# Kernel optimization log

Hardware: AMD Instinct MI355X
Metric: run time of the kernel (lower is better)

Reference implementation:

```python
import jax, jax.numpy as jnp
import numpy as np

B, S, D_MODEL, H = 2, 2048, 1024, 16
HD = D_MODEL // H  # 64
EPS = 1e-6


def setup_inputs() -> dict:
    key = jax.random.key(0)
    ks = jax.random.split(key, 8)
    x = jax.random.normal(ks[0], (B, S, D_MODEL), dtype=jnp.float32)
    # Proper RoPE rotation angles: theta_i = pos / 10000^(2i/head_dim)
    inv_freq = 1.0 / (10000.0 ** (np.arange(0, HD, 2, dtype=np.float32) / HD))  # (HD/2,)
    angles = np.arange(S, dtype=np.float32)[:, None] * inv_freq[None, :]        # (S, HD/2)
    rope_cos = jnp.asarray(np.cos(angles))
    rope_sin = jnp.asarray(np.sin(angles))
    w_std = 1.0 / np.sqrt(D_MODEL)
    wq = jax.random.normal(ks[1], (D_MODEL, D_MODEL), dtype=jnp.float32) * w_std
    wk = jax.random.normal(ks[2], (D_MODEL, D_MODEL), dtype=jnp.float32) * w_std
    wv = jax.random.normal(ks[3], (D_MODEL, D_MODEL), dtype=jnp.float32) * w_std
    wo = jax.random.normal(ks[4], (D_MODEL, D_MODEL), dtype=jnp.float32) * w_std
    q_scale = 1.0 + 0.02 * jax.random.normal(ks[5], (HD,), dtype=jnp.float32)
    k_scale = 1.0 + 0.02 * jax.random.normal(ks[6], (HD,), dtype=jnp.float32)
    return {"x": x, "wq": wq, "wk": wk, "wv": wv, "wo": wo,
            "q_scale": q_scale, "k_scale": k_scale,
            "rope_cos": rope_cos, "rope_sin": rope_sin}


def _rmsnorm(t, scale):
    # RMSNorm over head_dim
    var = jnp.mean(jnp.square(t), axis=-1, keepdims=True)
    return t * jax.lax.rsqrt(var + EPS) * scale


def _apply_rope(t, cos, sin):
    # t: (B,S,H,HD); interpret consecutive pairs as complex (real, imag)
    b, s, h, d = t.shape
    tp = t.reshape(b, s, h, d // 2, 2)
    tr, ti = tp[..., 0], tp[..., 1]
    c = cos[None, :, None, :]  # (1,S,1,HD/2)
    sn = sin[None, :, None, :]
    or_ = tr * c - ti * sn
    oi = tr * sn + ti * c
    return jnp.stack([or_, oi], axis=-1).reshape(b, s, h, d)


def reference(x, wq, wk, wv, wo, q_scale, k_scale, rope_cos, rope_sin):
    b, s, _ = x.shape
    # Torch-style linear: y = x @ W^T, W is (out, in)
    q = jnp.einsum('bsd,od->bso', x, wq).reshape(b, s, H, HD)
    k = jnp.einsum('bsd,od->bso', x, wk).reshape(b, s, H, HD)
    v = jnp.einsum('bsd,od->bso', x, wv).reshape(b, s, H, HD)
    q = _apply_rope(_rmsnorm(q, q_scale), rope_cos, rope_sin)
    k = _apply_rope(_rmsnorm(k, k_scale), rope_cos, rope_sin)
    # scaled dot-product attention (no mask), fp32 softmax
    scale = 1.0 / np.sqrt(HD)
    scores = jnp.einsum('bqhd,bkhd->bhqk', q, k) * scale
    probs = jax.nn.softmax(scores.astype(jnp.float32), axis=-1)
    attn = jnp.einsum('bhqk,bkhd->bqhd', probs, v).reshape(b, s, D_MODEL)
    return jnp.einsum('bso,do->bsd', attn, wo.T).astype(x.dtype) if False else jnp.einsum('bsd,od->bso', attn, wo)
```

## Files before the change

### kernel.cpp

```cpp
#include <hip/hip_runtime.h>
#include <hip/hip_bf16.h>


#define B_ 2
#define S_ 2048
#define D_ 1024
#define H_ 16
#define HD_ 64
#define M_ (B_*S_)

typedef __attribute__((ext_vector_type(8))) short short8;
typedef __attribute__((ext_vector_type(4))) short short4v;
typedef __attribute__((ext_vector_type(4))) float f32x4;
typedef __attribute__((ext_vector_type(4))) _Float16 half4;

static __device__ __forceinline__ short f2bf(float f) {
    __hip_bfloat16 h = __float2bfloat16(f);
    return *reinterpret_cast<short*>(&h);
}
static __device__ __forceinline__ short f2h(float f) {
    _Float16 h = (_Float16)f;
    return *reinterpret_cast<short*>(&h);
}
static __device__ __forceinline__ float h2f(short s) {
    _Float16 h; __builtin_memcpy(&h, &s, 2); return (float)h;
}
static __device__ __forceinline__ float bf2f(short s) {
    unsigned u = ((unsigned)(unsigned short)s) << 16;
    float f; __builtin_memcpy(&f, &u, 4); return f;
}

typedef __attribute__((address_space(1))) const unsigned int gu32_t;
typedef __attribute__((address_space(3))) unsigned int lu32_t;
static __device__ __forceinline__ void gld16(const short* g, short* l) {
    __builtin_amdgcn_global_load_lds((gu32_t*)g, (lu32_t*)l, 16, 0, 0);
}

__global__ __launch_bounds__(256)
void convert_bf16(const float* __restrict__ x,
                  const float* __restrict__ wq, const float* __restrict__ wk,
                  const float* __restrict__ wv, const float* __restrict__ wo,
                  short* __restrict__ xb, short* __restrict__ wqkvb, short* __restrict__ wob)
{
    const size_t t4 = ((size_t)blockIdx.x * 256 + threadIdx.x) * 4;
    const float* src; short* dst; size_t off, doff;
    if (t4 < 4194304)      { src = x;  dst = xb;    off = t4;           doff = t4; }
    else if (t4 < 5242880) { src = wq; dst = wqkvb; off = t4 - 4194304; doff = t4 - 4194304; }
    else if (t4 < 6291456) { src = wk; dst = wqkvb; off = t4 - 5242880; doff = t4 - 4194304; }
    else if (t4 < 7340032) { src = wv; dst = wqkvb; off = t4 - 6291456; doff = t4 - 4194304; }
    else                   { src = wo; dst = wob;   off = t4 - 7340032; doff = t4 - 7340032; }
    float4 v = *(const float4*)(src + off);
    short4v s = { f2bf(v.x), f2bf(v.y), f2bf(v.z), f2bf(v.w) };
    *(short4v*)(dst + doff) = s;
}

__global__ __launch_bounds__(256)
void gemm_qkv(const short* __restrict__ A, const short* __restrict__ Bw,
              short* __restrict__ Qb, short* __restrict__ Kb, short* __restrict__ Vt)
{
    __shared__ __align__(16) short As[128*32];
    __shared__ __align__(16) short Bs[128*32];
    const int tid = threadIdx.x;
    const int w = tid >> 6, lane = tid & 63, quad = lane >> 4, l16 = lane & 15;
    const int wr = w >> 1, wc = w & 1;
    const int bm0 = blockIdx.x * 128, bn0 = blockIdx.y * 128;

    const int srow = tid >> 2;
    const int skch = (tid & 3) * 8;
    const short* gA0 = A  + (size_t)(bm0 + srow) * 1024 + skch;
    const short* gA1 = A  + (size_t)(bm0 + 64 + srow) * 1024 + skch;
    const short* gB0 = Bw + (size_t)(bn0 + srow) * 1024 + skch;
    const short* gB1 = Bw + (size_t)(bn0 + 64 + srow) * 1024 + skch;
    short* lA0 = As + w*512;
    short* lA1 = As + 2048 + w*512;
    short* lB0 = Bs + w*512;
    short* lB1 = Bs + 2048 + w*512;

    f32x4 acc[4][4];
    #pragma unroll
    for (int i = 0; i < 4; ++i)
        #pragma unroll
        for (int j = 0; j < 4; ++j) acc[i][j] = (f32x4){0.f,0.f,0.f,0.f};

    for (int k0 = 0; k0 < 1024; k0 += 32) {
        __syncthreads();
        gld16(gA0 + k0, lA0);
        gld16(gA1 + k0, lA1);
        gld16(gB0 + k0, lB0);
        gld16(gB1 + k0, lB1);
        __syncthreads();
        short8 af[4], bfr[4];
        #pragma unroll
        for (int i = 0; i < 4; ++i)
            af[i] = *(const short8*)(As + (wr*64 + i*16 + l16)*32 + quad*8);
        #pragma unroll
        for (int j = 0; j < 4; ++j)
            bfr[j] = *(const short8*)(Bs + (wc*64 + j*16 + l16)*32 + quad*8);
        #pragma unroll
        for (int i = 0; i < 4; ++i)
            #pragma unroll
            for (int j = 0; j < 4; ++j)
                acc[i][j] = __builtin_amdgcn_mfma_f32_16x16x32_bf16(af[i], bfr[j], acc[i][j], 0, 0, 0);
    }

    #pragma unroll
    for (int i = 0; i < 4; ++i) {
        #pragma unroll
        for (int r = 0; r < 4; ++r) {
            const int m = bm0 + wr*64 + i*16 + quad*4 + r;
            #pragma unroll
            for (int j = 0; j < 4; ++j) {
                const int n = bn0 + wc*64 + j*16 + l16;
                const float v = acc[i][j][r];
                const int which = n >> 10, nn = n & 1023;
                const int h = nn >> 6, hd = nn & 63;
                const int b = m >> 11, s = m & (S_-1);
                if (which == 0)      Qb[(((size_t)b*H_ + h)*S_ + s)*HD_ + hd] = f2bf(v);
                else if (which == 1) Kb[(((size_t)b*H_ + h)*S_ + s)*HD_ + hd] = f2bf(v);
                else                 Vt[(((size_t)b*H_ + h)*HD_ + hd)*S_ + s] = f2h(v);
            }
        }
    }
}

__global__ __launch_bounds__(256)
void gemm_out(const short* __restrict__ A, const short* __restrict__ Bw,
              float* __restrict__ C)
{
    __shared__ __align__(16) short As[64*32];
    __shared__ __align__(16) short Bs[128*32];
    const int tid = threadIdx.x;
    const int w = tid >> 6, lane = tid & 63, quad = lane >> 4, l16 = lane & 15;
    const int bm0 = blockIdx.x * 64, bn0 = blockIdx.y * 128;

    const int srow = tid >> 2;
    const int skch = (tid & 3) * 8;
    const short* gA  = A  + (size_t)(bm0 + srow) * 1024 + skch;
    const short* gB0 = Bw + (size_t)(bn0 + srow) * 1024 + skch;
    const short* gB1 = Bw + (size_t)(bn0 + 64 + srow) * 1024 + skch;
    short* lA  = As + w*512;
    short* lB0 = Bs + w*512;
    short* lB1 = Bs + 2048 + w*512;

    f32x4 acc[4][2];
    #pragma unroll
    for (int i = 0; i < 4; ++i) {
        acc[i][0] = (f32x4){0.f,0.f,0.f,0.f};
        acc[i][1] = (f32x4){0.f,0.f,0.f,0.f};
    }

    for (int k0 = 0; k0 < 1024; k0 += 32) {
        __syncthreads();
        gld16(gA  + k0, lA);
        gld16(gB0 + k0, lB0);
        gld16(gB1 + k0, lB1);
        __syncthreads();
        short8 af[4], bfr[2];
        #pragma unroll
        for (int i = 0; i < 4; ++i)
            af[i] = *(const short8*)(As + (i*16 + l16)*32 + quad*8);
        #pragma unroll
        for (int j = 0; j < 2; ++j)
            bfr[j] = *(const short8*)(Bs + (w*32 + j*16 + l16)*32 + quad*8);
        #pragma unroll
        for (int i = 0; i < 4; ++i)
            #pragma unroll
            for (int j = 0; j < 2; ++j)
                acc[i][j] = __builtin_amdgcn_mfma_f32_16x16x32_bf16(af[i], bfr[j], acc[i][j], 0, 0, 0);
    }

    #pragma unroll
    for (int i = 0; i < 4; ++i)
        #pragma unroll
        for (int r = 0; r < 4; ++r) {
            const int m = bm0 + i*16 + quad*4 + r;
            #pragma unroll
            for (int j = 0; j < 2; ++j) {
                const int n = bn0 + w*32 + j*16 + l16;
                C[(size_t)m*1024 + n] = acc[i][j][r];
            }
        }
}

__global__ __launch_bounds__(256)
void rmsnorm_rope(short* __restrict__ qbh, short* __restrict__ kbh,
                  const float* __restrict__ q_scale, const float* __restrict__ k_scale,
                  const float* __restrict__ rope_cos, const float* __restrict__ rope_sin)
{
    const int lane = threadIdx.x & 63;
    const int wid  = threadIdx.x >> 6;
    const int row  = blockIdx.x * 4 + wid;
    const bool isq = (blockIdx.y == 0);
    short* t = isq ? qbh : kbh;
    const float* sc = isq ? q_scale : k_scale;
    const int s = row & (S_-1);
    float v = bf2f(t[(size_t)row * HD_ + lane]);
    float ssum = v * v;
    #pragma unroll
    for (int m = 32; m >= 1; m >>= 1) ssum += __shfl_xor(ssum, m, 64);
    float r = rsqrtf(ssum * (1.0f/64.0f) + 1e-6f);
    float nv = v * r * sc[lane];
    const int p = lane >> 1;
    float c  = rope_cos[s*32 + p];
    float sn = rope_sin[s*32 + p];
    float partner = __shfl_xor(nv, 1, 64);
    float outv = (lane & 1) ? (partner * sn + nv * c) : (nv * c - partner * sn);
    if (isq) outv *= 0.18033688011112042f;
    t[(size_t)row * HD_ + lane] = f2bf(outv);
}

__global__ __launch_bounds__(256, 2)
void flash_mfma(const short* __restrict__ qb, const short* __restrict__ kb,
                const short* __restrict__ vt, short* __restrict__ po, float* __restrict__ pl)
{
    __shared__ __align__(16) short Ks[64*64];
    __shared__ __align__(16) short Vs[64*64];

    const int tid  = threadIdx.x;
    const int wv   = tid >> 6;
    const int lane = tid & 63;
    const int quad = lane >> 4;
    const int l16  = lane & 15;
    const int bh   = blockIdx.y;
    const int b    = bh >> 4, h = bh & (H_-1);
    const int q0   = blockIdx.x * 128 + wv * 32;
    const int sp   = blockIdx.z;
    const int kt0  = sp * 1024;
    const size_t hbase = (size_t)bh * S_ * HD_;
    const size_t vbase = (size_t)bh * HD_ * S_;
    short* po_sp = po + (size_t)sp * 4194304;
    float* pl_sp = pl + (size_t)sp * 65536;

    const int c0r = tid >> 3,       c0c = tid & 7;
    const int c1r = (tid+256) >> 3, c1c = (tid+256) & 7;

    short8 qfrag[2][2];
    #pragma unroll
    for (int qf = 0; qf < 2; ++qf)
        #pragma unroll
        for (int c = 0; c < 2; ++c)
            qfrag[qf][c] = *(const short8*)(qb + hbase + (size_t)(q0 + qf*16 + l16)*HD_ + c*32 + quad*8);

    f32x4 Oacc[2][4];
    #pragma unroll
    for (int qf = 0; qf < 2; ++qf)
        #pragma unroll
        for (int dt = 0; dt < 4; ++dt) Oacc[qf][dt] = (f32x4){0.f,0.f,0.f,0.f};
    float l_lane[2] = {0.f, 0.f};

    short8 rk0 = *(const short8*)(kb + hbase + (size_t)(kt0 + c0r)*HD_ + c0c*8);
    short8 rk1 = *(const short8*)(kb + hbase + (size_t)(kt0 + c1r)*HD_ + c1c*8);
    short8 rv0 = *(const short8*)(vt + vbase + (size_t)c0r*S_ + kt0 + c0c*8);
    short8 rv1 = *(const short8*)(vt + vbase + (size_t)c1r*S_ + kt0 + c1c*8);

    #pragma unroll 1
    for (int t = 0; t < 16; ++t) {
        __syncthreads();
        *(short8*)(Ks + c0r*64 + ((c0c ^ (c0r & 7)) << 3)) = rk0;
        *(short8*)(Ks + c1r*64 + ((c1c ^ (c1r & 7)) << 3)) = rk1;
        *(short8*)(Vs + c0r*64 + ((c0c ^ (c0r & 7)) << 3)) = rv0;
        *(short8*)(Vs + c1r*64 + ((c1c ^ (c1r & 7)) << 3)) = rv1;
        __syncthreads();
        if (t < 15) {
            const int ktn = kt0 + (t+1)*64;
            rk0 = *(const short8*)(kb + hbase + (size_t)(ktn + c0r)*HD_ + c0c*8);
            rk1 = *(const short8*)(kb + hbase + (size_t)(ktn + c1r)*HD_ + c1c*8);
            rv0 = *(const short8*)(vt + vbase + (size_t)c0r*S_ + ktn + c0c*8);
            rv1 = *(const short8*)(vt + vbase + (size_t)c1r*S_ + ktn + c1c*8);
        }

        #pragma unroll
        for (int st = 0; st < 4; ++st) {
            short8 kf0 = *(const short8*)(Ks + (st*16 + l16)*64 + (((quad    ) ^ (l16 & 7)) << 3));
            short8 kf1 = *(const short8*)(Ks + (st*16 + l16)*64 + (((4 + quad) ^ (l16 & 7)) << 3));
            #pragma unroll
            for (int qf = 0; qf < 2; ++qf) {
                f32x4 acc = (f32x4){0.f,0.f,0.f,0.f};
                acc = __builtin_amdgcn_mfma_f32_16x16x32_bf16(kf0, qfrag[qf][0], acc, 0, 0, 0);
                acc = __builtin_amdgcn_mfma_f32_16x16x32_bf16(kf1, qfrag[qf][1], acc, 0, 0, 0);
                half4 pb;
                #pragma unroll
                for (int r = 0; r < 4; ++r) {
                    float p = __builtin_amdgcn_exp2f(acc[r] - 12.0f);
                    l_lane[qf] += p;
                    pb[r] = (_Float16)p;
                }
                const int ch16 = st*2 + (quad >> 1);
                const int sw   = ((ch16 ^ (l16 & 7)) << 3) + (quad & 1)*4;
                #pragma unroll
                for (int dt = 0; dt < 4; ++dt) {
                    half4 va = *(const half4*)(Vs + (dt*16 + l16)*64 + sw);
                    Oacc[qf][dt] = __builtin_amdgcn_mfma_f32_16x16x16f16(va, pb, Oacc[qf][dt], 0, 0, 0);
                }
            }
        }
    }

    #pragma unroll
    for (int qf = 0; qf < 2; ++qf) {
        l_lane[qf] += __shfl_xor(l_lane[qf], 16, 64);
        l_lane[qf] += __shfl_xor(l_lane[qf], 32, 64);
        if (quad == 0) pl_sp[(size_t)bh*S_ + q0 + qf*16 + l16] = l_lane[qf];
    }
    #pragma unroll
    for (int qf = 0; qf < 2; ++qf) {
        const int s = q0 + qf*16 + l16;
        #pragma unroll
        for (int dt = 0; dt < 4; ++dt) {
            short4v o;
            #pragma unroll
            for (int r = 0; r < 4; ++r) o[r] = f2h(Oacc[qf][dt][r]);
            *(short4v*)(po_sp + (((size_t)b*S_ + s)*H_ + h)*HD_ + dt*16 + quad*4) = o;
        }
    }
}

__global__ __launch_bounds__(256)
void flash_combine(const short* __restrict__ po, const float* __restrict__ pl,
                   short* __restrict__ attnb)
{
    const size_t idx4 = ((size_t)blockIdx.x * 256 + threadIdx.x) * 4;
    const size_t row  = idx4 >> 6;
    const int h  = (int)(row & 15);
    const size_t bs = row >> 4;
    const int b  = (int)(bs >> 11);
    const int s  = (int)(bs & (S_-1));
    const int bh = b*16 + h;
    const float l = pl[(size_t)bh*S_ + s] + pl[65536 + (size_t)bh*S_ + s];
    const float inv = 1.0f / l;
    short4v a0 = *(const short4v*)(po + idx4);
    short4v a1 = *(const short4v*)(po + 4194304 + idx4);
    short4v o;
    #pragma unroll
    for (int i = 0; i < 4; ++i) o[i] = f2bf((h2f(a0[i]) + h2f(a1[i])) * inv);
    *(short4v*)(attnb + idx4) = o;
}

extern "C" void kernel_launch(void* const* d_in, const int* in_sizes, int n_in,
                              void* d_out, int out_size, void* d_ws, size_t ws_size,
                              hipStream_t stream)
{
    (void)in_sizes; (void)n_in; (void)out_size; (void)ws_size;
    const float* x        = (const float*)d_in[0];
    const float* wq       = (const float*)d_in[1];
    const float* wk       = (const float*)d_in[2];
    const float* wv       = (const float*)d_in[3];
    const float* wo       = (const float*)d_in[4];
    const float* q_scale  = (const float*)d_in[5];
    const float* k_scale  = (const float*)d_in[6];
    const float* rope_cos = (const float*)d_in[7];
    const float* rope_sin = (const float*)d_in[8];
    float* out = (float*)d_out;
    short* ws  = (short*)d_ws;

    short* qbh   = ws;
    short* kbh   = ws + 4194304;
    short* vt    = ws + 8388608;
    short* attnb = ws + 12582912;
    short* xb    = ws + 16777216;
    short* wqkvb = ws + 20971520;
    short* wob   = ws + 24117248;
    short* po    = ws + 25165824;
    float* pl    = (float*)(ws + 33554432);

    convert_bf16<<<dim3(8192), 256, 0, stream>>>(x, wq, wk, wv, wo, xb, wqkvb, wob);
    gemm_qkv<<<dim3(M_/128, 24), 256, 0, stream>>>(xb, wqkvb, qbh, kbh, vt);
    rmsnorm_rope<<<dim3(B_*H_*S_/4, 2), 256, 0, stream>>>(qbh, kbh, q_scale, k_scale, rope_cos, rope_sin);
    flash_mfma<<<dim3(S_/128, B_*H_, 2), 256, 0, stream>>>(qbh, kbh, vt, po, pl);
    flash_combine<<<dim3(4096), 256, 0, stream>>>(po, pl, attnb);
    gemm_out<<<dim3(M_/64, D_/128), 256, 0, stream>>>(attnb, wob, out);
}
```

Measured before the change: 225.7 us.

## Fuse split-K attention combine into output projection GEMM, hoist V fragment loads

Removes the separate flash_combine kernel and folds its normalisation into gemm_out's A-tile staging. Each thread loads the two fp16 partial outputs, sums them, scales by the precomputed inverse row sums, and writes bf16 into LDS. This saves one launch and the attnb round trip through memory. The cost is that the A tile now goes through registers instead of the async global_load_lds path, and each thread does 16 pl reads per block, with the po tile re-read by every column block. In the flash kernel, the V fragments are loaded once per st and reused across both q fragments rather than reloaded per qf.

```diff
diff --git a/kernel.cpp b/kernel.cpp
--- a/kernel.cpp
+++ b/kernel.cpp
@@ -13,6 +13,7 @@
 typedef __attribute__((ext_vector_type(4))) short short4v;
 typedef __attribute__((ext_vector_type(4))) float f32x4;
 typedef __attribute__((ext_vector_type(4))) _Float16 half4;
+typedef __attribute__((ext_vector_type(8))) _Float16 half8;
 
 static __device__ __forceinline__ short f2bf(float f) {
     __hip_bfloat16 h = __float2bfloat16(f);
@@ -21,9 +22,6 @@
 static __device__ __forceinline__ short f2h(float f) {
     _Float16 h = (_Float16)f;
     return *reinterpret_cast<short*>(&h);
-}
-static __device__ __forceinline__ float h2f(short s) {
-    _Float16 h; __builtin_memcpy(&h, &s, 2); return (float)h;
 }
 static __device__ __forceinline__ float bf2f(short s) {
     unsigned u = ((unsigned)(unsigned short)s) << 16;
@@ -124,8 +122,8 @@
 }
 
 __global__ __launch_bounds__(256)
-void gemm_out(const short* __restrict__ A, const short* __restrict__ Bw,
-              float* __restrict__ C)
+void gemm_out(const short* __restrict__ po, const float* __restrict__ pl,
+              const short* __restrict__ Bw, float* __restrict__ C)
 {
     __shared__ __align__(16) short As[64*32];
     __shared__ __align__(16) short Bs[128*32];
@@ -135,12 +133,17 @@
 
     const int srow = tid >> 2;
     const int skch = (tid & 3) * 8;
-    const short* gA  = A  + (size_t)(bm0 + srow) * 1024 + skch;
+    const int m = bm0 + srow;
+    const int b = m >> 11, s = m & (S_-1);
     const short* gB0 = Bw + (size_t)(bn0 + srow) * 1024 + skch;
     const short* gB1 = Bw + (size_t)(bn0 + 64 + srow) * 1024 + skch;
-    short* lA  = As + w*512;
     short* lB0 = Bs + w*512;
     short* lB1 = Bs + 2048 + w*512;
+
+    float inv[16];
+    #pragma unroll
+    for (int h = 0; h < 16; ++h)
+        inv[h] = 1.0f / (pl[((size_t)(b*16 + h))*S_ + s] + pl[65536 + ((size_t)(b*16 + h))*S_ + s]);
 
     f32x4 acc[4][2];
     #pragma unroll
@@ -150,8 +153,15 @@
     }
 
     for (int k0 = 0; k0 < 1024; k0 += 32) {
-        __syncthreads();
-        gld16(gA  + k0, lA);
+        const int h = k0 >> 6;
+        half8 p0 = *(const half8*)(po +            (size_t)m*1024 + k0 + skch);
+        half8 p1 = *(const half8*)(po + 4194304 + (size_t)m*1024 + k0 + skch);
+        short8 a;
+        #pragma unroll
+        for (int j = 0; j < 8; ++j)
+            a[j] = f2bf(((float)p0[j] + (float)p1[j]) * inv[h]);
+        __syncthreads();
+        *(short8*)(As + srow*32 + skch) = a;
         gld16(gB0 + k0, lB0);
         gld16(gB1 + k0, lB1);
         __syncthreads();
@@ -173,11 +183,11 @@
     for (int i = 0; i < 4; ++i)
         #pragma unroll
         for (int r = 0; r < 4; ++r) {
-            const int m = bm0 + i*16 + quad*4 + r;
+            const int mm = bm0 + i*16 + quad*4 + r;
             #pragma unroll
             for (int j = 0; j < 2; ++j) {
                 const int n = bn0 + w*32 + j*16 + l16;
-                C[(size_t)m*1024 + n] = acc[i][j][r];
+                C[(size_t)mm*1024 + n] = acc[i][j][r];
             }
         }
 }
@@ -273,6 +283,12 @@
         for (int st = 0; st < 4; ++st) {
             short8 kf0 = *(const short8*)(Ks + (st*16 + l16)*64 + (((quad    ) ^ (l16 & 7)) << 3));
             short8 kf1 = *(const short8*)(Ks + (st*16 + l16)*64 + (((4 + quad) ^ (l16 & 7)) << 3));
+            const int ch16 = st*2 + (quad >> 1);
+            const int sw   = ((ch16 ^ (l16 & 7)) << 3) + (quad & 1)*4;
+            half4 va[4];
+            #pragma unroll
+            for (int dt = 0; dt < 4; ++dt)
+                va[dt] = *(const half4*)(Vs + (dt*16 + l16)*64 + sw);
             #pragma unroll
             for (int qf = 0; qf < 2; ++qf) {
                 f32x4 acc = (f32x4){0.f,0.f,0.f,0.f};
@@ -285,13 +301,9 @@
                     l_lane[qf] += p;
                     pb[r] = (_Float16)p;
                 }
-                const int ch16 = st*2 + (quad >> 1);
-                const int sw   = ((ch16 ^ (l16 & 7)) << 3) + (quad & 1)*4;
                 #pragma unroll
-                for (int dt = 0; dt < 4; ++dt) {
-                    half4 va = *(const half4*)(Vs + (dt*16 + l16)*64 + sw);
-                    Oacc[qf][dt] = __builtin_amdgcn_mfma_f32_16x16x16f16(va, pb, Oacc[qf][dt], 0, 0, 0);
-                }
+                for (int dt = 0; dt < 4; ++dt)
+                    Oacc[qf][dt] = __builtin_amdgcn_mfma_f32_16x16x16f16(va[dt], pb, Oacc[qf][dt], 0, 0, 0);
             }
         }
     }
@@ -313,27 +325,6 @@
             *(short4v*)(po_sp + (((size_t)b*S_ + s)*H_ + h)*HD_ + dt*16 + quad*4) = o;
         }
     }
-}
-
-__global__ __launch_bounds__(256)
-void flash_combine(const short* __restrict__ po, const float* __restrict__ pl,
-                   short* __restrict__ attnb)
-{
-    const size_t idx4 = ((size_t)blockIdx.x * 256 + threadIdx.x) * 4;
-    const size_t row  = idx4 >> 6;
-    const int h  = (int)(row & 15);
-    const size_t bs = row >> 4;
-    const int b  = (int)(bs >> 11);
-    const int s  = (int)(bs & (S_-1));
-    const int bh = b*16 + h;
-    const float l = pl[(size_t)bh*S_ + s] + pl[65536 + (size_t)bh*S_ + s];
-    const float inv = 1.0f / l;
-    short4v a0 = *(const short4v*)(po + idx4);
-    short4v a1 = *(const short4v*)(po + 4194304 + idx4);
-    short4v o;
-    #pragma unroll
-    for (int i = 0; i < 4; ++i) o[i] = f2bf((h2f(a0[i]) + h2f(a1[i])) * inv);
-    *(short4v*)(attnb + idx4) = o;
 }
 
 extern "C" void kernel_launch(void* const* d_in, const int* in_sizes, int n_in,
@@ -356,7 +347,6 @@
     short* qbh   = ws;
     short* kbh   = ws + 4194304;
     short* vt    = ws + 8388608;
-    short* attnb = ws + 12582912;
     short* xb    = ws + 16777216;
     short* wqkvb = ws + 20971520;
     short* wob   = ws + 24117248;
@@ -367,6 +357,5 @@
     gemm_qkv<<<dim3(M_/128, 24), 256, 0, stream>>>(xb, wqkvb, qbh, kbh, vt);
     rmsnorm_rope<<<dim3(B_*H_*S_/4, 2), 256, 0, stream>>>(qbh, kbh, q_scale, k_scale, rope_cos, rope_sin);
     flash_mfma<<<dim3(S_/128, B_*H_, 2), 256, 0, stream>>>(qbh, kbh, vt, po, pl);
-    flash_combine<<<dim3(4096), 256, 0, stream>>>(po, pl, attnb);
-    gemm_out<<<dim3(M_/64, D_/128), 256, 0, stream>>>(attnb, wob, out);
-}
+    gemm_out<<<dim3(M_/64, D_/128), 256, 0, stream>>>(po, pl, wob, out);
+}
```

Result: no change. 222.6 us (-1.4%).
